# Optimization experiments

Hardware: AMD Instinct MI355X
Metric: run time of the kernel (lower is better)

## Reference

```python
import jax, jax.numpy as jnp
import numpy as np

N = 524288      # number of evaluation points (particles)
NMODE = 8       # number of eikonal modes
NCOEF = 6       # Gauss-Hermite coefficients per mode (full h00..h02 branch)
NFIELD = 2      # fields: (phi, A_parallel)
NPSI = 512      # psi interpolation grid size
K = 3           # alpha branches from the Clebsch mapping (2*pi shifts)
R0 = 1.7        # major radius for the theta stand-in mapping
DX = 1.0 / (NPSI - 1)
TWO_PI = 2.0 * np.pi


def cubic_interp(xq, table):
    """Catmull-Rom cubic interpolation on a uniform grid over [0, 1].
    xq: [N]; table: [NPSI] or [NPSI, Nmode]. Returns [N] or [N, Nmode]."""
    npts = table.shape[0]
    s = xq / jnp.asarray(DX, xq.dtype)
    i = jnp.clip(jnp.floor(s).astype(jnp.int32), 1, npts - 3)
    tt = s - i.astype(xq.dtype)
    tt = tt.reshape(tt.shape + (1,) * (table.ndim - 1))  # broadcast over trailing dims
    fm1, f0, f1, f2 = table[i - 1], table[i], table[i + 1], table[i + 2]
    t2 = tt * tt
    t3 = t2 * tt
    wm1 = 0.5 * (-t3 + 2.0 * t2 - tt)
    w0 = 0.5 * (3.0 * t3 - 5.0 * t2 + 2.0)
    w1 = 0.5 * (-3.0 * t3 + 4.0 * t2 + tt)
    w2 = 0.5 * (t3 - t2)
    return wm1 * fm1 + w0 * f0 + w1 * f1 + w2 * f2


def _hermite_poly(c, x, y, h20, h11, h02):
    """c: [M, 6, F] (real or imag part); x: [N, M]; y/h11/h02: [N, M, K].
    Returns p: [N, M, K, F] = sum_j c_j * H_j(x, y)."""
    return (c[None, :, None, 0, :]
            + c[:, 1, :][None, :, None, :] * x[:, :, None, None]
            + c[:, 2, :][None, :, None, :] * y[..., None]
            + c[:, 3, :][None, :, None, :] * h20[:, :, None, None]
            + c[:, 4, :][None, :, None, :] * h11[..., None]
            + c[:, 5, :][None, :, None, :] * h02[..., None])


def _forward(t, r, varphi, z, psi, gh_re, gh_im, alpha0_table, iota_table,
             psi0, psi_scale, alpha_scale, omega, n):
    theta = jnp.arctan2(z, r - R0)                                   # [N]
    iota = cubic_interp(psi, iota_table)                             # [N]
    alpha0 = cubic_interp(psi, alpha0_table)                         # [N, M]
    shifts = jnp.asarray([-TWO_PI, 0.0, TWO_PI], dtype=psi.dtype)    # [K]
    alpha = iota[:, None] * (theta[:, None] + shifts[None, :])       # [N, K]

    x = (psi[:, None] - psi0) / psi_scale                            # [N, M]
    y = (alpha[:, None, :] - alpha0[:, :, None]) / alpha_scale[None, :, None]  # [N, M, K]
    g = jnp.exp(-0.5 * (jnp.square(x)[..., None] + jnp.square(y)))   # [N, M, K]

    h20 = 4.0 * jnp.square(x) - 2.0                                  # [N, M]
    h11 = x[..., None] * y                                           # [N, M, K]
    h02 = 4.0 * jnp.square(y) - 2.0                                  # [N, M, K]

    p_re = _hermite_poly(gh_re, x, y, h20, h11, h02)                 # [N, M, K, F]
    p_im = _hermite_poly(gh_im, x, y, h20, h11, h02)                 # [N, M, K, F]

    nf = n.astype(psi.dtype)
    phase = (omega[None, :, None] * t
             - nf[None, :, None] * (varphi[:, None, None]
                                    - (alpha[:, None, :] - alpha0[:, :, None])))  # [N, M, K]

    ev = (jnp.einsum('nmkf,nmk->nf', p_re, g * jnp.cos(phase))
          - jnp.einsum('nmkf,nmk->nf', p_im, g * jnp.sin(phase)))    # [N, F]
    return ev


def setup_inputs() -> dict:
    key = jax.random.key(0)
    ks = jax.random.split(key, 14)
    t = jax.random.uniform(ks[0], (), jnp.float32) * 10.0
    r = R0 + (jax.random.uniform(ks[1], (N,), jnp.float32) - 0.5)          # around major radius
    varphi = jax.random.uniform(ks[2], (N,), jnp.float32) * TWO_PI
    z = (jax.random.uniform(ks[3], (N,), jnp.float32) - 0.5)
    psi = 0.05 + 0.9 * jax.random.uniform(ks[4], (N,), jnp.float32)        # stay interior to grid
    gh_re = jax.random.normal(ks[5], (NMODE, NCOEF, NFIELD), jnp.float32) * 0.5
    gh_im = jax.random.normal(ks[6], (NMODE, NCOEF, NFIELD), jnp.float32) * 0.5
    alpha0_table = jax.random.normal(ks[7], (NPSI, NMODE), jnp.float32) * 0.1
    iota_table = 1.0 + 0.5 * jax.random.uniform(ks[8], (NPSI,), jnp.float32)
    psi0 = 0.2 + 0.6 * jax.random.uniform(ks[9], (NMODE,), jnp.float32)
    psi_scale = 0.05 + 0.1 * jax.random.uniform(ks[10], (NMODE,), jnp.float32)
    alpha_scale = 0.4 + 0.4 * jax.random.uniform(ks[11], (NMODE,), jnp.float32)
    omega = jax.random.normal(ks[12], (NMODE,), jnp.float32)
    n = jax.random.randint(ks[13], (NMODE,), 1, 20, jnp.int32)
    return {"t": t, "r": r, "varphi": varphi, "z": z, "psi": psi,
            "gh_re": gh_re, "gh_im": gh_im, "alpha0_table": alpha0_table,
            "iota_table": iota_table, "psi0": psi0, "psi_scale": psi_scale,
            "alpha_scale": alpha_scale, "omega": omega, "n": n}


def reference(t, r, varphi, z, psi, gh_re, gh_im, alpha0_table, iota_table,
              psi0, psi_scale, alpha_scale, omega, n):
    return _forward(t, r, varphi, z, psi, gh_re, gh_im, alpha0_table,
                    iota_table, psi0, psi_scale, alpha_scale, omega, n)
```

## Files before the change

### kernel.cpp

```cpp
#include <hip/hip_runtime.h>

#define NMODE   8
#define NPSI    512
#define RSTRIDE 12

__global__ __launch_bounds__(256, 4) void eik_kernel(
    const float* __restrict__ t_p,
    const float* __restrict__ r_p,
    const float* __restrict__ vp_p,
    const float* __restrict__ z_p,
    const float* __restrict__ psi_p,
    const float* __restrict__ ghre_p,
    const float* __restrict__ ghim_p,
    const float* __restrict__ a0tab_p,
    const float* __restrict__ iotatab_p,
    const float* __restrict__ psi0_p,
    const float* __restrict__ psisc_p,
    const float* __restrict__ alsc_p,
    const float* __restrict__ omega_p,
    const int*   __restrict__ nmode_p,
    float* __restrict__ out,
    int npart)
{
    constexpr float R0      = 1.7f;
    constexpr float TWO_PI  = 6.28318530717958647692f;
    constexpr float INV_2PI = 0.15915494309189533577f;
    constexpr float NHL2E   = -0.72134752044448170368f;

    __shared__ float s_pack[NPSI][RSTRIDE];

    const int tid = threadIdx.x;
    const int i   = blockIdx.x * 256 + tid;
    const bool live = (i < npart);

    float ps = 0.f, th = 0.f, vp = 0.f;
    if (live) {
        ps = psi_p[i];
        th = atan2f(z_p[i], r_p[i] - R0);
        vp = vp_p[i];
    }

    const float s = ps * (float)(NPSI - 1);
    int ii = (int)floorf(s);
    ii = ii < 1 ? 1 : (ii > NPSI - 3 ? NPSI - 3 : ii);
    const float tt = s - (float)ii;
    const float t2 = tt * tt, t3 = t2 * tt;
    float w[4];
    w[0] = 0.5f * (-t3 + 2.0f * t2 - tt);
    w[1] = 0.5f * (3.0f * t3 - 5.0f * t2 + 2.0f);
    w[2] = 0.5f * (-3.0f * t3 + 4.0f * t2 + tt);
    w[3] = 0.5f * (t3 - t2);

    for (int p = tid; p < NPSI; p += 256) {
        const float4* src = reinterpret_cast<const float4*>(a0tab_p + p * 8);
        const float4 lo = src[0];
        const float4 hi = src[1];
        const float  io = iotatab_p[p];
        float* dst = s_pack[p];
        *reinterpret_cast<float4*>(dst)     = lo;
        *reinterpret_cast<float4*>(dst + 4) = hi;
        dst[8] = io;
    }
    __syncthreads();

    if (!live) return;

    float a0v[NMODE];
    #pragma unroll
    for (int q = 0; q < NMODE; ++q) a0v[q] = 0.0f;
    float iotv = 0.0f;

    #pragma unroll
    for (int j = 0; j < 4; ++j) {
        const float* rowp = s_pack[ii - 1 + j];
        const float4 lo = *reinterpret_cast<const float4*>(rowp);
        const float4 hi = *reinterpret_cast<const float4*>(rowp + 4);
        const float  io = rowp[8];
        const float  wj = w[j];
        a0v[0] = fmaf(wj, lo.x, a0v[0]);
        a0v[1] = fmaf(wj, lo.y, a0v[1]);
        a0v[2] = fmaf(wj, lo.z, a0v[2]);
        a0v[3] = fmaf(wj, lo.w, a0v[3]);
        a0v[4] = fmaf(wj, hi.x, a0v[4]);
        a0v[5] = fmaf(wj, hi.y, a0v[5]);
        a0v[6] = fmaf(wj, hi.z, a0v[6]);
        a0v[7] = fmaf(wj, hi.w, a0v[7]);
        iotv   = fmaf(wj, io,   iotv);
    }

    const float tval = t_p[0];
    const float at   = iotv * th;
    const float dyb  = iotv * TWO_PI;

    float acc0 = 0.0f, acc1 = 0.0f;

    #pragma unroll
    for (int m = 0; m < NMODE; ++m) {
        const float c0r0 = ghre_p[m*12+ 0], c0r1 = ghre_p[m*12+ 1];
        const float c1r0 = ghre_p[m*12+ 2], c1r1 = ghre_p[m*12+ 3];
        const float c2r0 = ghre_p[m*12+ 4], c2r1 = ghre_p[m*12+ 5];
        const float c3r0 = ghre_p[m*12+ 6], c3r1 = ghre_p[m*12+ 7];
        const float c4r0 = ghre_p[m*12+ 8], c4r1 = ghre_p[m*12+ 9];
        const float c5r0 = ghre_p[m*12+10], c5r1 = ghre_p[m*12+11];
        const float c0i0 = ghim_p[m*12+ 0], c0i1 = ghim_p[m*12+ 1];
        const float c1i0 = ghim_p[m*12+ 2], c1i1 = ghim_p[m*12+ 3];
        const float c2i0 = ghim_p[m*12+ 4], c2i1 = ghim_p[m*12+ 5];
        const float c3i0 = ghim_p[m*12+ 6], c3i1 = ghim_p[m*12+ 7];
        const float c4i0 = ghim_p[m*12+ 8], c4i1 = ghim_p[m*12+ 9];
        const float c5i0 = ghim_p[m*12+10], c5i1 = ghim_p[m*12+11];
        const float psi0m = psi0_p[m];
        const float ipsc  = __builtin_amdgcn_rcpf(psisc_p[m]);
        const float iasc  = __builtin_amdgcn_rcpf(alsc_p[m]);
        const float ot    = omega_p[m] * tval;
        const float nf    = (float)nmode_p[m];

        const float a0    = a0v[m];
        const float x     = (ps - psi0m) * ipsc;
        const float xx    = x * x;
        const float h20   = fmaf(4.0f, xx, -2.0f);
        const float xterm = xx * NHL2E;
        const float base  = at - a0;
        const float y1    = base * iasc;
        const float dy    = dyb * iasc;
        const float pcr   = (ot - nf * (vp - base)) * INV_2PI;
        const float dpr   = nf * iotv;

        const float pxr0 = fmaf(c3r0, h20, fmaf(c1r0, x, c0r0));
        const float pxr1 = fmaf(c3r1, h20, fmaf(c1r1, x, c0r1));
        const float pxi0 = fmaf(c3i0, h20, fmaf(c1i0, x, c0i0));
        const float pxi1 = fmaf(c3i1, h20, fmaf(c1i1, x, c0i1));
        const float er0  = fmaf(c4r0, x, c2r0);
        const float er1  = fmaf(c4r1, x, c2r1);
        const float ei0  = fmaf(c4i0, x, c2i0);
        const float ei1  = fmaf(c4i1, x, c2i1);

        #pragma unroll
        for (int k = 0; k < 3; ++k) {
            const float kf  = (float)(k - 1);
            const float y   = fmaf(kf, dy, y1);
            const float phr = fmaf(kf, dpr, pcr);
            const float yy  = y * y;
            const float g   = __builtin_amdgcn_exp2f(fmaf(yy, NHL2E, xterm));
            const float fr  = __builtin_amdgcn_fractf(phr);
            const float sn  = __builtin_amdgcn_sinf(fr);
            const float cs  = __builtin_amdgcn_cosf(fr);
            const float h02 = fmaf(4.0f, yy, -2.0f);
            const float pr0 = fmaf(c5r0, h02, fmaf(er0, y, pxr0));
            const float pr1 = fmaf(c5r1, h02, fmaf(er1, y, pxr1));
            const float pi0 = fmaf(c5i0, h02, fmaf(ei0, y, pxi0));
            const float pi1 = fmaf(c5i1, h02, fmaf(ei1, y, pxi1));
            const float gc = g * cs;
            const float gs = g * sn;
            acc0 = fmaf(pr0, gc, acc0); acc0 = fmaf(pi0, -gs, acc0);
            acc1 = fmaf(pr1, gc, acc1); acc1 = fmaf(pi1, -gs, acc1);
        }
    }

    reinterpret_cast<float2*>(out)[i] = make_float2(acc0, acc1);
}

extern "C" void kernel_launch(void* const* d_in, const int* in_sizes, int n_in,
                              void* d_out, int out_size, void* d_ws, size_t ws_size,
                              hipStream_t stream) {
    const float* t      = (const float*)d_in[0];
    const float* r      = (const float*)d_in[1];
    const float* varphi = (const float*)d_in[2];
    const float* z      = (const float*)d_in[3];
    const float* psi    = (const float*)d_in[4];
    const float* gh_re  = (const float*)d_in[5];
    const float* gh_im  = (const float*)d_in[6];
    const float* a0t    = (const float*)d_in[7];
    const float* iot    = (const float*)d_in[8];
    const float* psi0   = (const float*)d_in[9];
    const float* psc    = (const float*)d_in[10];
    const float* asc    = (const float*)d_in[11];
    const float* omg    = (const float*)d_in[12];
    const int*   nn     = (const int*)d_in[13];
    float* out = (float*)d_out;

    const int npart  = in_sizes[1];
    const int blocks = (npart + 255) / 256;
    eik_kernel<<<blocks, 256, 0, stream>>>(t, r, varphi, z, psi, gh_re, gh_im,
                                           a0t, iot, psi0, psc, asc, omg, nn,
                                           out, npart);
}
```

Baseline: 96.88 us.

## Drop LDS table staging, use angle-addition for phase branches, split accumulators

Removes the per-block shared-memory copy of the alpha0/iota tables and the barrier, and reads the four interpolation rows straight from global memory (cache-resident) instead. It replaces the three per-branch sin/cos evaluations with two sin/cos pairs combined by angle-addition identities, cutting the transcendental count per mode. It also splits the accumulators so the two FMA chains per output are independent. The direct global gathers may cost more latency than the LDS reads did, and the identity-based phases can lose some accuracy for large phase arguments.

```diff
diff --git a/kernel.cpp b/kernel.cpp
--- a/kernel.cpp
+++ b/kernel.cpp
@@ -1,10 +1,9 @@
 #include <hip/hip_runtime.h>
 
-#define NMODE   8
-#define NPSI    512
-#define RSTRIDE 12
+#define NMODE 8
+#define NPSI  512
 
-__global__ __launch_bounds__(256, 4) void eik_kernel(
+__global__ __launch_bounds__(256) void eik_kernel(
     const float* __restrict__ t_p,
     const float* __restrict__ r_p,
     const float* __restrict__ vp_p,
@@ -27,72 +26,52 @@
     constexpr float INV_2PI = 0.15915494309189533577f;
     constexpr float NHL2E   = -0.72134752044448170368f;
 
-    __shared__ float s_pack[NPSI][RSTRIDE];
+    const int i = blockIdx.x * 256 + threadIdx.x;
+    if (i >= npart) return;
 
-    const int tid = threadIdx.x;
-    const int i   = blockIdx.x * 256 + tid;
-    const bool live = (i < npart);
+    const float ps   = psi_p[i];
+    const float rr   = r_p[i];
+    const float zz   = z_p[i];
+    const float vp   = vp_p[i];
+    const float tval = t_p[0];
 
-    float ps = 0.f, th = 0.f, vp = 0.f;
-    if (live) {
-        ps = psi_p[i];
-        th = atan2f(z_p[i], r_p[i] - R0);
-        vp = vp_p[i];
-    }
+    const float th = atan2f(zz, rr - R0);
 
     const float s = ps * (float)(NPSI - 1);
     int ii = (int)floorf(s);
     ii = ii < 1 ? 1 : (ii > NPSI - 3 ? NPSI - 3 : ii);
     const float tt = s - (float)ii;
     const float t2 = tt * tt, t3 = t2 * tt;
-    float w[4];
-    w[0] = 0.5f * (-t3 + 2.0f * t2 - tt);
-    w[1] = 0.5f * (3.0f * t3 - 5.0f * t2 + 2.0f);
-    w[2] = 0.5f * (-3.0f * t3 + 4.0f * t2 + tt);
-    w[3] = 0.5f * (t3 - t2);
+    const float w0 = 0.5f * (-t3 + 2.0f * t2 - tt);
+    const float w1 = 0.5f * (3.0f * t3 - 5.0f * t2 + 2.0f);
+    const float w2 = 0.5f * (-3.0f * t3 + 4.0f * t2 + tt);
+    const float w3 = 0.5f * (t3 - t2);
 
-    for (int p = tid; p < NPSI; p += 256) {
-        const float4* src = reinterpret_cast<const float4*>(a0tab_p + p * 8);
-        const float4 lo = src[0];
-        const float4 hi = src[1];
-        const float  io = iotatab_p[p];
-        float* dst = s_pack[p];
-        *reinterpret_cast<float4*>(dst)     = lo;
-        *reinterpret_cast<float4*>(dst + 4) = hi;
-        dst[8] = io;
-    }
-    __syncthreads();
-
-    if (!live) return;
+    const float4* a0q = reinterpret_cast<const float4*>(a0tab_p);
+    const int r0 = ii - 1;
+    const float4 lo0 = a0q[2*(r0+0)+0], hi0 = a0q[2*(r0+0)+1];
+    const float4 lo1 = a0q[2*(r0+1)+0], hi1 = a0q[2*(r0+1)+1];
+    const float4 lo2 = a0q[2*(r0+2)+0], hi2 = a0q[2*(r0+2)+1];
+    const float4 lo3 = a0q[2*(r0+3)+0], hi3 = a0q[2*(r0+3)+1];
+    const float io0 = iotatab_p[r0+0], io1 = iotatab_p[r0+1];
+    const float io2 = iotatab_p[r0+2], io3 = iotatab_p[r0+3];
 
     float a0v[NMODE];
-    #pragma unroll
-    for (int q = 0; q < NMODE; ++q) a0v[q] = 0.0f;
-    float iotv = 0.0f;
+    a0v[0] = w0*lo0.x + w1*lo1.x + w2*lo2.x + w3*lo3.x;
+    a0v[1] = w0*lo0.y + w1*lo1.y + w2*lo2.y + w3*lo3.y;
+    a0v[2] = w0*lo0.z + w1*lo1.z + w2*lo2.z + w3*lo3.z;
+    a0v[3] = w0*lo0.w + w1*lo1.w + w2*lo2.w + w3*lo3.w;
+    a0v[4] = w0*hi0.x + w1*hi1.x + w2*hi2.x + w3*hi3.x;
+    a0v[5] = w0*hi0.y + w1*hi1.y + w2*hi2.y + w3*hi3.y;
+    a0v[6] = w0*hi0.z + w1*hi1.z + w2*hi2.z + w3*hi3.z;
+    a0v[7] = w0*hi0.w + w1*hi1.w + w2*hi2.w + w3*hi3.w;
+    const float iotv = w0*io0 + w1*io1 + w2*io2 + w3*io3;
 
-    #pragma unroll
-    for (int j = 0; j < 4; ++j) {
-        const float* rowp = s_pack[ii - 1 + j];
-        const float4 lo = *reinterpret_cast<const float4*>(rowp);
-        const float4 hi = *reinterpret_cast<const float4*>(rowp + 4);
-        const float  io = rowp[8];
-        const float  wj = w[j];
-        a0v[0] = fmaf(wj, lo.x, a0v[0]);
-        a0v[1] = fmaf(wj, lo.y, a0v[1]);
-        a0v[2] = fmaf(wj, lo.z, a0v[2]);
-        a0v[3] = fmaf(wj, lo.w, a0v[3]);
-        a0v[4] = fmaf(wj, hi.x, a0v[4]);
-        a0v[5] = fmaf(wj, hi.y, a0v[5]);
-        a0v[6] = fmaf(wj, hi.z, a0v[6]);
-        a0v[7] = fmaf(wj, hi.w, a0v[7]);
-        iotv   = fmaf(wj, io,   iotv);
-    }
+    const float at  = iotv * th;
+    const float dyb = iotv * TWO_PI;
 
-    const float tval = t_p[0];
-    const float at   = iotv * th;
-    const float dyb  = iotv * TWO_PI;
-
-    float acc0 = 0.0f, acc1 = 0.0f;
+    float acc0a = 0.0f, acc0b = 0.0f;
+    float acc1a = 0.0f, acc1b = 0.0f;
 
     #pragma unroll
     for (int m = 0; m < NMODE; ++m) {
@@ -125,6 +104,15 @@
         const float pcr   = (ot - nf * (vp - base)) * INV_2PI;
         const float dpr   = nf * iotv;
 
+        const float snC = __builtin_amdgcn_sinf(__builtin_amdgcn_fractf(pcr));
+        const float csC = __builtin_amdgcn_cosf(__builtin_amdgcn_fractf(pcr));
+        const float snD = __builtin_amdgcn_sinf(__builtin_amdgcn_fractf(dpr));
+        const float csD = __builtin_amdgcn_cosf(__builtin_amdgcn_fractf(dpr));
+        const float pcc = csC * csD, pss = snC * snD;
+        const float psc_ = snC * csD, pcs = csC * snD;
+        const float csM = pcc + pss, snM = psc_ - pcs;
+        const float csP = pcc - pss, snP = psc_ + pcs;
+
         const float pxr0 = fmaf(c3r0, h20, fmaf(c1r0, x, c0r0));
         const float pxr1 = fmaf(c3r1, h20, fmaf(c1r1, x, c0r1));
         const float pxi0 = fmaf(c3i0, h20, fmaf(c1i0, x, c0i0));
@@ -136,14 +124,12 @@
 
         #pragma unroll
         for (int k = 0; k < 3; ++k) {
-            const float kf  = (float)(k - 1);
-            const float y   = fmaf(kf, dy, y1);
-            const float phr = fmaf(kf, dpr, pcr);
+            const float kf = (float)(k - 1);
+            const float y  = fmaf(kf, dy, y1);
+            const float cs = (k == 0) ? csM : (k == 1) ? csC : csP;
+            const float sn = (k == 0) ? snM : (k == 1) ? snC : snP;
             const float yy  = y * y;
             const float g   = __builtin_amdgcn_exp2f(fmaf(yy, NHL2E, xterm));
-            const float fr  = __builtin_amdgcn_fractf(phr);
-            const float sn  = __builtin_amdgcn_sinf(fr);
-            const float cs  = __builtin_amdgcn_cosf(fr);
             const float h02 = fmaf(4.0f, yy, -2.0f);
             const float pr0 = fmaf(c5r0, h02, fmaf(er0, y, pxr0));
             const float pr1 = fmaf(c5r1, h02, fmaf(er1, y, pxr1));
@@ -151,12 +137,14 @@
             const float pi1 = fmaf(c5i1, h02, fmaf(ei1, y, pxi1));
             const float gc = g * cs;
             const float gs = g * sn;
-            acc0 = fmaf(pr0, gc, acc0); acc0 = fmaf(pi0, -gs, acc0);
-            acc1 = fmaf(pr1, gc, acc1); acc1 = fmaf(pi1, -gs, acc1);
+            acc0a = fmaf(pr0, gc, acc0a);
+            acc0b = fmaf(pi0, gs, acc0b);
+            acc1a = fmaf(pr1, gc, acc1a);
+            acc1b = fmaf(pi1, gs, acc1b);
         }
     }
 
-    reinterpret_cast<float2*>(out)[i] = make_float2(acc0, acc1);
+    reinterpret_cast<float2*>(out)[i] = make_float2(acc0a - acc0b, acc1a - acc1b);
 }
 
 extern "C" void kernel_launch(void* const* d_in, const int* in_sizes, int n_in,
```

After: 98.38 us. Within noise of the previous version (+1.5%).
